# Performance work log

Measured on AMD Instinct MI355X. Metric: run time of the kernel, lower is better.

Reference implementation:

```python
import jax, jax.numpy as jnp
import numpy as np

N_NODES = 100000
N_EDGES = 1600000
IN_C, HID_C, OUT_C = 512, 128, 40


def gcn_conv(x, edge_index):
    """Symmetric-normalized sparse aggregation: out[d] = sum_e 1/sqrt(deg[s]*deg[d]) * x[s]."""
    n = x.shape[0]
    src, dst = edge_index[0], edge_index[1]
    deg = jax.ops.segment_sum(jnp.ones_like(dst, dtype=x.dtype), dst, num_segments=n)
    deg = jnp.maximum(deg, 1.0)  # guard isolated nodes
    dinv = jax.lax.rsqrt(deg)
    w = dinv[src] * dinv[dst]                      # [E]
    msg = x[src] * w[:, None]                      # [E, C] gather + scale
    return jax.ops.segment_sum(msg, dst, num_segments=n)  # scatter-add -> [N, C]


def setup_inputs() -> dict:
    key = jax.random.key(0)
    k1, k2, k3, k4 = jax.random.split(key, 4)
    x = jax.random.normal(k1, (N_NODES, IN_C), dtype=jnp.float32)
    edge_index = jax.random.randint(k2, (2, N_EDGES), 0, N_NODES, dtype=jnp.int64)
    # xavier_uniform with gain=1.414 (as in reset_parameters), zero biases
    def xavier(k, shape, gain=1.414):
        fan_out, fan_in = shape
        bound = gain * np.sqrt(6.0 / (fan_in + fan_out))
        return jax.random.uniform(k, shape, jnp.float32, -bound, bound)
    W0 = xavier(k3, (HID_C, IN_C))
    b0 = jnp.zeros((HID_C,), jnp.float32)
    W1 = xavier(k4, (OUT_C, HID_C))
    b1 = jnp.zeros((OUT_C,), jnp.float32)
    return {"x": x, "edge_index": edge_index, "W0": W0, "b0": b0, "W1": W1, "b1": b1}


def reference(x, edge_index, W0, b0, W1, b1):
    # layer 0: project -> sparse aggregate -> bias -> relu (dropout off in eval)
    h = x @ W0.T
    h = gcn_conv(h, edge_index)
    h = jax.nn.relu(h + b0)
    # final layer: project -> sparse aggregate -> bias (no activation)
    h = h @ W1.T
    h = gcn_conv(h, edge_index)
    return h + b1
```

## Files before the change

kernel.cpp:

```cpp
#include <hip/hip_runtime.h>
#include <hip/hip_bf16.h>
#include <cstddef>

#define N_NODES 100000
#define N_EDGES 1600000
#define IN_C 512
#define HID_C 128
#define OUT_C 40
#define OUT_CP 48
#define EPB 8000
#define NPART 200
#define NBKT 196
#define BSHIFT 9

typedef short bf16x8 __attribute__((ext_vector_type(8)));
typedef float f32x4 __attribute__((ext_vector_type(4)));

__device__ __forceinline__ float bf2f(unsigned short u) {
    union { unsigned int i; float f; } v; v.i = ((unsigned int)u) << 16; return v.f;
}
__device__ __forceinline__ float bf2f_lo(unsigned int u) {
    union { unsigned int i; float f; } v; v.i = u << 16; return v.f;
}
__device__ __forceinline__ float bf2f_hi(unsigned int u) {
    union { unsigned int i; float f; } v; v.i = u & 0xFFFF0000u; return v.f;
}
__device__ __forceinline__ unsigned short f2bf(float f) {
    union { float f; unsigned int i; } v; v.f = f;
    unsigned int x = v.i;
    return (unsigned short)((x + 0x7FFFu + ((x >> 16) & 1u)) >> 16);
}

__device__ __forceinline__ void glds16(const void* g, void* l) {
    __builtin_amdgcn_global_load_lds(
        (const __attribute__((address_space(1))) unsigned int*)g,
        (__attribute__((address_space(3))) unsigned int*)l,
        16, 0, 0);
}

__global__ void k_detect(const unsigned int* __restrict__ xbits,
                         const int* __restrict__ ei32, int* __restrict__ flags) {
    int lane = threadIdx.x & 63;
    unsigned int b = xbits[lane * 33 + 1];
    int e = (int)((b >> 23) & 0xFFu);
    unsigned long long bal = __ballot(e >= 90 && e <= 160);
    int zpred = (lane < 8) ? (ei32[2 * lane + 1] == 0) : 0;
    unsigned long long zb = __ballot(zpred);
    if (lane == 0) {
        flags[0] = (__popcll(bal) >= 32) ? 0 : 1;
        flags[1] = ((zb & 0xFFull) == 0xFFull) ? 1 : 0;
    }
}

__device__ __forceinline__ int load_src(const int* ei, int mi, int e) {
    return mi ? ei[2 * e] : ei[e];
}
__device__ __forceinline__ int load_dst(const int* ei, int mi, int e) {
    return mi ? ei[2 * (N_EDGES + e)] : ei[N_EDGES + e];
}

#define NW_TOTAL (IN_C * HID_C + HID_C * OUT_C + HID_C + OUT_C)
__global__ void k_norm_w(const void* __restrict__ W0, const void* __restrict__ W1,
                         const void* __restrict__ b0, const void* __restrict__ b1,
                         const int* __restrict__ flags,
                         unsigned short* __restrict__ w0n, unsigned short* __restrict__ w1n,
                         float* __restrict__ b0n, float* __restrict__ b1n) {
    int mf = flags[0];
    int i = blockIdx.x * 256 + threadIdx.x;
    if (i >= NW_TOTAL) return;
    if (i < IN_C * HID_C) {
        w0n[i] = mf ? ((const unsigned short*)W0)[i] : f2bf(((const float*)W0)[i]);
    } else if (i < IN_C * HID_C + HID_C * OUT_C) {
        int j = i - IN_C * HID_C;
        w1n[j] = mf ? ((const unsigned short*)W1)[j] : f2bf(((const float*)W1)[j]);
    } else if (i < IN_C * HID_C + HID_C * OUT_C + HID_C) {
        int j = i - IN_C * HID_C - HID_C * OUT_C;
        b0n[j] = mf ? bf2f(((const unsigned short*)b0)[j]) : ((const float*)b0)[j];
    } else {
        int j = i - IN_C * HID_C - HID_C * OUT_C - HID_C;
        b1n[j] = mf ? bf2f(((const unsigned short*)b1)[j]) : ((const float*)b1)[j];
    }
}

__global__ __launch_bounds__(256) void k_part1(const int* __restrict__ ei,
                                               const int* __restrict__ flags,
                                               int* __restrict__ bcnt,
                                               int* __restrict__ block_off) {
    __shared__ int h[NBKT];
    int t = threadIdx.x;
    for (int i = t; i < NBKT; i += 256) h[i] = 0;
    __syncthreads();
    int mi = flags[1];
    int base = blockIdx.x * EPB;
    for (int j = t; j < EPB; j += 256) {
        int e = base + j;
        if (e < N_EDGES) atomicAdd(&h[load_dst(ei, mi, e) >> BSHIFT], 1);
    }
    __syncthreads();
    for (int i = t; i < NBKT; i += 256)
        block_off[blockIdx.x * NBKT + i] = atomicAdd(&bcnt[i], h[i]);
}

__global__ void k_scan_bkt(const int* __restrict__ bcnt, int* __restrict__ bbase) {
    __shared__ int sm[256];
    int t = threadIdx.x;
    int v = (t < NBKT) ? bcnt[t] : 0;
    sm[t] = v; __syncthreads();
    for (int off = 1; off < 256; off <<= 1) {
        int a = (t >= off) ? sm[t - off] : 0;
        __syncthreads();
        sm[t] += a;
        __syncthreads();
    }
    if (t < NBKT) bbase[t] = sm[t] - v;
    if (t == NBKT - 1) bbase[NBKT] = sm[t];
}

__global__ __launch_bounds__(256) void k_part2(const int* __restrict__ ei,
                                               const int* __restrict__ flags,
                                               const int* __restrict__ bbase,
                                               const int* __restrict__ block_off,
                                               unsigned int* __restrict__ bedges) {
    __shared__ int cur[NBKT];
    int t = threadIdx.x;
    for (int i = t; i < NBKT; i += 256)
        cur[i] = bbase[i] + block_off[blockIdx.x * NBKT + i];
    __syncthreads();
    int mi = flags[1];
    int base = blockIdx.x * EPB;
    for (int j = t; j < EPB; j += 256) {
        int e = base + j;
        if (e < N_EDGES) {
            int d = load_dst(ei, mi, e);
            int s = load_src(ei, mi, e);
            int p = atomicAdd(&cur[d >> BSHIFT], 1);
            bedges[p] = ((unsigned int)s << BSHIFT) | (unsigned int)(d & 511);
        }
    }
}

__global__ __launch_bounds__(512) void k_bucket_csr(const unsigned int* __restrict__ bedges,
                                                    const int* __restrict__ bbase,
                                                    int* __restrict__ rowptr,
                                                    float* __restrict__ dinv,
                                                    int* __restrict__ col) {
    __shared__ int cnt[512];
    __shared__ int cur[512];
    int b = blockIdx.x, t = threadIdx.x;
    int ebeg = bbase[b], eend = bbase[b + 1];
    cnt[t] = 0;
    __syncthreads();
    for (int j = ebeg + t; j < eend; j += 512)
        atomicAdd(&cnt[bedges[j] & 511], 1);
    __syncthreads();
    int v = cnt[t];
    cur[t] = v; __syncthreads();
    for (int off = 1; off < 512; off <<= 1) {
        int a = (t >= off) ? cur[t - off] : 0;
        __syncthreads();
        cur[t] += a;
        __syncthreads();
    }
    int excl = cur[t] - v;
    int node = b * 512 + t;
    if (node < N_NODES) {
        rowptr[node] = ebeg + excl;
        float dd = (float)v; if (dd < 1.f) dd = 1.f;
        dinv[node] = rsqrtf(dd);
    } else if (node == N_NODES) {
        rowptr[N_NODES] = ebeg + excl;
    }
    __syncthreads();
    cur[t] = ebeg + excl;
    __syncthreads();
    for (int j = ebeg + t; j < eend; j += 512) {
        unsigned int pk = bedges[j];
        int p = atomicAdd(&cur[pk & 511], 1);
        col[p] = (int)(pk >> BSHIFT);
    }
}

#define G1_BUF 24576
#define G1_BOFF 16384

__device__ __forceinline__ void gemm1_f32_async(const float* __restrict__ xg,
                                                const unsigned short* __restrict__ w0n,
                                                const float* __restrict__ dinv,
                                                unsigned short* __restrict__ h1,
                                                char* __restrict__ smem,
                                                int node0, int t) {
    const int w = t >> 6;
    const int lane = t & 63;
    const int r16 = lane & 15;
    const int quad = lane >> 4;

    f32x4 acc[2][8];
#pragma unroll
    for (int m = 0; m < 2; m++)
#pragma unroll
        for (int c = 0; c < 8; c++) acc[m][c] = (f32x4){0.f, 0.f, 0.f, 0.f};

    const int lrow = lane >> 3;
    const int lch = (lane & 7) ^ lrow;
    const float* pa[4];
#pragma unroll
    for (int g = 0; g < 4; g++) {
        int r = node0 + w * 32 + 8 * g + lrow;
        if (r >= N_NODES) r = N_NODES - 1;
        pa[g] = xg + (size_t)r * IN_C + lch * 4;
    }
    const unsigned short* pb[2];
#pragma unroll
    for (int g = 0; g < 2; g++)
        pb[g] = w0n + (size_t)((2 * w + g) * 16 + r16) * IN_C + quad * 8;

    auto stage = [&](int buf, int ks) {
        char* Ab = smem + buf * G1_BUF + w * 4096;
        char* Bb = smem + buf * G1_BUF + G1_BOFF + w * 2048;
        glds16(pa[0] + ks, Ab);
        glds16(pa[1] + ks, Ab + 1024);
        glds16(pa[2] + ks, Ab + 2048);
        glds16(pa[3] + ks, Ab + 3072);
        glds16(pb[0] + ks, Bb);
        glds16(pb[1] + ks, Bb + 1024);
    };

    const int swz = r16 & 7;

    auto compute = [&](int buf) {
        const char* Ab = smem + buf * G1_BUF;
        const char* Bb = Ab + G1_BOFF;
        bf16x8 a[2];
#pragma unroll
        for (int m = 0; m < 2; m++) {
            int rowb = (w * 32 + m * 16 + r16) * 128;
            int c0 = ((2 * quad) ^ swz) * 16;
            int c1 = ((2 * quad + 1) ^ swz) * 16;
            float4 fa = *reinterpret_cast<const float4*>(Ab + rowb + c0);
            float4 fb = *reinterpret_cast<const float4*>(Ab + rowb + c1);
            a[m] = (bf16x8){(short)f2bf(fa.x), (short)f2bf(fa.y), (short)f2bf(fa.z), (short)f2bf(fa.w),
                            (short)f2bf(fb.x), (short)f2bf(fb.y), (short)f2bf(fb.z), (short)f2bf(fb.w)};
        }
#pragma unroll
        for (int ct = 0; ct < 8; ct++) {
            bf16x8 b = *reinterpret_cast<const bf16x8*>(Bb + ct * 1024 + lane * 16);
            acc[0][ct] = __builtin_amdgcn_mfma_f32_16x16x32_bf16(a[0], b, acc[0][ct], 0, 0, 0);
            acc[1][ct] = __builtin_amdgcn_mfma_f32_16x16x32_bf16(a[1], b, acc[1][ct], 0, 0, 0);
        }
    };

    stage(0, 0);
    stage(1, 32);
    for (int tt = 0; tt < 14; ++tt) {
        asm volatile("s_waitcnt vmcnt(6)" ::: "memory");
        __builtin_amdgcn_sched_barrier(0);
        __builtin_amdgcn_s_barrier();
        compute(tt & 1);
        __builtin_amdgcn_s_barrier();
        stage(tt & 1, (tt + 2) * 32);
    }
    asm volatile("s_waitcnt vmcnt(6)" ::: "memory");
    __builtin_amdgcn_sched_barrier(0);
    __builtin_amdgcn_s_barrier();
    compute(0);
    asm volatile("s_waitcnt vmcnt(0)" ::: "memory");
    __builtin_amdgcn_sched_barrier(0);
    __builtin_amdgcn_s_barrier();
    compute(1);

#pragma unroll
    for (int m = 0; m < 2; m++) {
#pragma unroll
        for (int r = 0; r < 4; r++) {
            int row = node0 + w * 32 + m * 16 + quad * 4 + r;
            if (row < N_NODES) {
                float dv = dinv[row];
#pragma unroll
                for (int ct = 0; ct < 8; ct++)
                    h1[(size_t)row * HID_C + ct * 16 + r16] = f2bf(acc[m][ct][r] * dv);
            }
        }
    }
}

__device__ __forceinline__ void gemm1_bf16_async(const unsigned short* __restrict__ xg,
                                                 const unsigned short* __restrict__ w0n,
                                                 const float* __restrict__ dinv,
                                                 unsigned short* __restrict__ h1,
                                                 unsigned short* __restrict__ smem,
                                                 int node0, int t) {
    const int w = t >> 6;
    const int lane = t & 63;
    const int r16 = lane & 15;
    const int quad = lane >> 4;

    f32x4 acc[2][8];
#pragma unroll
    for (int m = 0; m < 2; m++)
#pragma unroll
        for (int c = 0; c < 8; c++) acc[m][c] = (f32x4){0.f, 0.f, 0.f, 0.f};

    int rA0 = node0 + (2 * w) * 16 + r16;     if (rA0 >= N_NODES) rA0 = N_NODES - 1;
    int rA1 = node0 + (2 * w + 1) * 16 + r16; if (rA1 >= N_NODES) rA1 = N_NODES - 1;
    const unsigned short* pa0 = xg + (size_t)rA0 * IN_C + quad * 8;
    const unsigned short* pa1 = xg + (size_t)rA1 * IN_C + quad * 8;
    const unsigned short* pb0 = w0n + (size_t)((2 * w) * 16 + r16) * IN_C + quad * 8;
    const unsigned short* pb1 = w0n + (size_t)((2 * w + 1) * 16 + r16) * IN_C + quad * 8;

    auto stage = [&](int buf, int ks) {
        unsigned short* a = smem + buf * 8192 + (2 * w) * 512;
        glds16(pa0 + ks, a);
        glds16(pa1 + ks, a + 512);
        glds16(pb0 + ks, a + 4096);
        glds16(pb1 + ks, a + 4096 + 512);
    };

    const int fo = quad * 128 + r16 * 8;

    auto compute = [&](int buf) {
        const unsigned short* Ab = smem + buf * 8192;
        const unsigned short* Bb = Ab + 4096;
        bf16x8 a0 = *reinterpret_cast<const bf16x8*>(Ab + (2 * w) * 512 + fo);
        bf16x8 a1 = *reinterpret_cast<const bf16x8*>(Ab + (2 * w + 1) * 512 + fo);
#pragma unroll
        for (int ct = 0; ct < 8; ct++) {
            bf16x8 b = *reinterpret_cast<const bf16x8*>(Bb + ct * 512 + fo);
            acc[0][ct] = __builtin_amdgcn_mfma_f32_16x16x32_bf16(a0, b, acc[0][ct], 0, 0, 0);
            acc[1][ct] = __builtin_amdgcn_mfma_f32_16x16x32_bf16(a1, b, acc[1][ct], 0, 0, 0);
        }
    };

    stage(0, 0);
    __syncthreads();
    for (int tt = 0; tt < 15; ++tt) {
        int cur = tt & 1;
        stage(cur ^ 1, (tt + 1) * 32);
        compute(cur);
        __syncthreads();
    }
    compute(1);

#pragma unroll
    for (int m = 0; m < 2; m++) {
#pragma unroll
        for (int r = 0; r < 4; r++) {
            int row = node0 + w * 32 + m * 16 + quad * 4 + r;
            if (row < N_NODES) {
                float dv = dinv[row];
#pragma unroll
                for (int ct = 0; ct < 8; ct++)
                    h1[(size_t)row * HID_C + ct * 16 + r16] = f2bf(acc[m][ct][r] * dv);
            }
        }
    }
}

__global__ __launch_bounds__(256, 3) void k_gemm1(const void* __restrict__ x,
                                                  const unsigned short* __restrict__ w0n,
                                                  const int* __restrict__ flags,
                                                  const float* __restrict__ dinv,
                                                  unsigned short* __restrict__ h1) {
    __shared__ __align__(16) char smem[2 * G1_BUF];
    int node0 = blockIdx.x * 128;
    int t = threadIdx.x;
    if (flags[0]) gemm1_bf16_async((const unsigned short*)x, w0n, dinv, h1,
                                   (unsigned short*)smem, node0, t);
    else          gemm1_f32_async((const float*)x, w0n, dinv, h1, smem, node0, t);
}

__global__ __launch_bounds__(256) void k_agg1g2(const int* __restrict__ rowptr,
                                                const int* __restrict__ col,
                                                const float* __restrict__ dinv,
                                                const unsigned int* __restrict__ h1v,
                                                const float* __restrict__ b0n,
                                                const unsigned short* __restrict__ w1p,
                                                float* __restrict__ p2) {
    __shared__ unsigned int H[16][68];
    int w = threadIdx.x >> 6;
    int lane = threadIdx.x & 63;
    int nb = blockIdx.x * 16;
    float bl = b0n[2 * lane], bh = b0n[2 * lane + 1];
#pragma unroll
    for (int i = 0; i < 4; i++) {
        int d = nb + w * 4 + i;
        int beg = __builtin_amdgcn_readfirstlane(rowptr[d]);
        int end = __builtin_amdgcn_readfirstlane(rowptr[d + 1]);
        float a0 = 0.f, a1 = 0.f;
        for (int j0 = beg; j0 < end; j0 += 16) {
            int s[16];
            float m[16];
#pragma unroll
            for (int q = 0; q < 16; q++) {
                int jj = j0 + q;
                int jc = jj < end ? jj : end - 1;
                s[q] = col[jc];
                m[q] = jj < end ? 1.f : 0.f;
            }
            unsigned int r[16];
#pragma unroll
            for (int q = 0; q < 16; q++) {
                const unsigned int* rp = h1v + (size_t)s[q] * 64;
                r[q] = rp[lane];
            }
#pragma unroll
            for (int q = 0; q < 16; q++) {
                a0 += m[q] * bf2f_lo(r[q]);
                a1 += m[q] * bf2f_hi(r[q]);
            }
        }
        float dv = dinv[d];
        float o0 = a0 * dv + bl;
        float o1 = a1 * dv + bh;
        o0 = o0 > 0.f ? o0 : 0.f;
        o1 = o1 > 0.f ? o1 : 0.f;
        H[w * 4 + i][lane] = (unsigned int)f2bf(o0) | ((unsigned int)f2bf(o1) << 16);
    }
    __syncthreads();
    if (w != 0) return;

    int r16 = lane & 15;
    int quad = lane >> 4;
    f32x4 acc[3];
#pragma unroll
    for (int c = 0; c < 3; c++) acc[c] = (f32x4){0.f, 0.f, 0.f, 0.f};

    const unsigned short* brow = w1p + (size_t)r16 * HID_C + quad * 8;
#pragma unroll
    for (int k0 = 0; k0 < HID_C; k0 += 32) {
        bf16x8 a = *reinterpret_cast<const bf16x8*>(&H[r16][k0 / 2 + quad * 4]);
#pragma unroll
        for (int ct = 0; ct < 3; ct++) {
            bf16x8 b = *reinterpret_cast<const bf16x8*>(brow + (size_t)ct * 16 * HID_C + k0);
            acc[ct] = __builtin_amdgcn_mfma_f32_16x16x32_bf16(a, b, acc[ct], 0, 0, 0);
        }
    }

    float dvv[4];
#pragma unroll
    for (int r = 0; r < 4; r++) dvv[r] = dinv[nb + quad * 4 + r];

#pragma unroll
    for (int ct = 0; ct < 3; ct++) {
        int chan = ct * 16 + r16;
        if (chan < OUT_C) {
#pragma unroll
            for (int r = 0; r < 4; r++) {
                p2[(size_t)(nb + quad * 4 + r) * OUT_C + chan] = acc[ct][r] * dvv[r];
            }
        }
    }
}

__global__ __launch_bounds__(256) void k_agg2(const int* __restrict__ rowptr,
                                              const int* __restrict__ col,
                                              const float* __restrict__ dinv,
                                              const float* __restrict__ p2,
                                              const float* __restrict__ b1n,
                                              const int* __restrict__ flags,
                                              void* __restrict__ out) {
    int w = threadIdx.x >> 6;
    int lane = threadIdx.x & 63;
    int d = blockIdx.x * 4 + w;
    if (d >= N_NODES || lane >= OUT_C) return;
    int beg = __builtin_amdgcn_readfirstlane(rowptr[d]);
    int end = __builtin_amdgcn_readfirstlane(rowptr[d + 1]);
    float acc = 0.f;
    for (int j0 = beg; j0 < end; j0 += 16) {
        int s[16];
        float m[16];
#pragma unroll
        for (int q = 0; q < 16; q++) {
            int jj = j0 + q;
            int jc = jj < end ? jj : end - 1;
            s[q] = col[jc];
            m[q] = jj < end ? 1.f : 0.f;
        }
        float r[16];
#pragma unroll
        for (int q = 0; q < 16; q++) {
            const float* rp = p2 + (size_t)s[q] * OUT_C;
            r[q] = rp[lane];
        }
#pragma unroll
        for (int q = 0; q < 16; q++) acc += m[q] * r[q];
    }
    float v = acc * dinv[d] + b1n[lane];
    size_t idx = (size_t)d * OUT_C + lane;
    if (flags[0]) ((unsigned short*)out)[idx] = f2bf(v);
    else          ((float*)out)[idx] = v;
}

extern "C" void kernel_launch(void* const* d_in, const int* in_sizes, int n_in,
                              void* d_out, int out_size, void* d_ws, size_t ws_size,
                              hipStream_t stream) {
    const void* x  = d_in[0];
    const int* ei  = (const int*)d_in[1];
    const void* W0 = d_in[2];
    const void* b0 = d_in[3];
    const void* W1 = d_in[4];
    const void* b1 = d_in[5];

    char* ws = (char*)d_ws;
    size_t off = 0;
    auto alloc = [&](size_t bytes) {
        char* p = ws + off;
        off += (bytes + 511) & ~(size_t)511;
        return p;
    };
    int*   flags   = (int*)  alloc(sizeof(int) * 2);
    int*   rowptr  = (int*)  alloc(sizeof(int) * (N_NODES + 1));
    float* dinv    = (float*)alloc(sizeof(float) * N_NODES);
    int*   col     = (int*)  alloc(sizeof(int) * N_EDGES);
    int*   bcnt    = (int*)  alloc(sizeof(int) * NBKT);
    int*   bbase   = (int*)  alloc(sizeof(int) * (NBKT + 1));
    int*   bloff   = (int*)  alloc(sizeof(int) * NPART * NBKT);
    unsigned int* bedges = (unsigned int*)alloc(sizeof(unsigned int) * N_EDGES);
    unsigned short* w0n = (unsigned short*)alloc(sizeof(unsigned short) * IN_C * HID_C);
    unsigned short* w1n = (unsigned short*)alloc(sizeof(unsigned short) * OUT_CP * HID_C);
    float* b0n = (float*)alloc(sizeof(float) * HID_C);
    float* b1n = (float*)alloc(sizeof(float) * OUT_C);
    unsigned short* h1 = (unsigned short*)alloc(sizeof(unsigned short) * (size_t)N_NODES * HID_C);
    float* p2 = (float*)alloc(sizeof(float) * (size_t)N_NODES * OUT_C);

    k_detect<<<1, 64, 0, stream>>>((const unsigned int*)x, ei, flags);
    hipMemsetAsync(w1n, 0, sizeof(unsigned short) * OUT_CP * HID_C, stream);
    k_norm_w<<<(NW_TOTAL + 255) / 256, 256, 0, stream>>>(W0, W1, b0, b1, flags, w0n, w1n, b0n, b1n);

    hipMemsetAsync(bcnt, 0, sizeof(int) * NBKT, stream);
    k_part1<<<NPART, 256, 0, stream>>>(ei, flags, bcnt, bloff);
    k_scan_bkt<<<1, 256, 0, stream>>>(bcnt, bbase);
    k_part2<<<NPART, 256, 0, stream>>>(ei, flags, bbase, bloff, bedges);
    k_bucket_csr<<<NBKT, 512, 0, stream>>>(bedges, bbase, rowptr, dinv, col);

    k_gemm1<<<(N_NODES + 127) / 128, 256, 0, stream>>>(x, w0n, flags, dinv, h1);
    k_agg1g2<<<N_NODES / 16, 256, 0, stream>>>(rowptr, col, dinv,
                                               (const unsigned int*)h1, b0n,
                                               w1n, p2);
    k_agg2<<<(N_NODES + 3) / 4, 256, 0, stream>>>(rowptr, col, dinv, p2, b1n, flags, d_out);
}
```

Baseline: 493.4 us.

## Split gemm1 over output column halves, keep W0 slice resident in LDS

The first projection GEMM now launches two blocks per 128-row tile, each computing 64 output channels. Each block loads its full 64x512 bf16 slice of W0 into swizzled LDS once, then streams A operands straight from global memory into registers with a one-step software prefetch. This drops the double-buffered LDS staging of A and the per-step barriers. The trade-off is that each block rereads its x rows (fp32 or bf16) from global memory, doubling x traffic unless L2 absorbs it. It also uses 64 KB of LDS per block, so launch bounds drop to two blocks per CU.

```diff
diff --git a/kernel.cpp b/kernel.cpp
--- a/kernel.cpp
+++ b/kernel.cpp
@@ -12,6 +12,7 @@
 #define NPART 200
 #define NBKT 196
 #define BSHIFT 9
+#define G1_ROWBLK 782
 
 typedef short bf16x8 __attribute__((ext_vector_type(8)));
 typedef float f32x4 __attribute__((ext_vector_type(4)));
@@ -29,6 +30,10 @@
     union { float f; unsigned int i; } v; v.f = f;
     unsigned int x = v.i;
     return (unsigned short)((x + 0x7FFFu + ((x >> 16) & 1u)) >> 16);
+}
+__device__ __forceinline__ bf16x8 pack8(float4 a, float4 b) {
+    return (bf16x8){(short)f2bf(a.x), (short)f2bf(a.y), (short)f2bf(a.z), (short)f2bf(a.w),
+                    (short)f2bf(b.x), (short)f2bf(b.y), (short)f2bf(b.z), (short)f2bf(b.w)};
 }
 
 __device__ __forceinline__ void glds16(const void* g, void* l) {
@@ -180,93 +185,91 @@
     }
 }
 
-#define G1_BUF 24576
-#define G1_BOFF 16384
-
-__device__ __forceinline__ void gemm1_f32_async(const float* __restrict__ xg,
-                                                const unsigned short* __restrict__ w0n,
-                                                const float* __restrict__ dinv,
-                                                unsigned short* __restrict__ h1,
-                                                char* __restrict__ smem,
-                                                int node0, int t) {
+__device__ __forceinline__ const bf16x8* ldsB(const unsigned short* Bs, int row,
+                                              int s, int quad) {
+    int ch = (4 * s + quad) ^ (row & 7);
+    return reinterpret_cast<const bf16x8*>(
+        (const char*)Bs + row * 1024 + ch * 16);
+}
+
+template <int MF>
+__device__ __forceinline__ void gemm1_body(const void* __restrict__ x,
+                                           const unsigned short* __restrict__ w0n,
+                                           const float* __restrict__ dinv,
+                                           unsigned short* __restrict__ h1,
+                                           unsigned short* __restrict__ Bs,
+                                           int node0, int chb, int t) {
     const int w = t >> 6;
     const int lane = t & 63;
     const int r16 = lane & 15;
     const int quad = lane >> 4;
 
-    f32x4 acc[2][8];
+    {
+        const unsigned short* src = w0n + (size_t)(chb + 16 * w) * IN_C;
+        unsigned short* dst = Bs + (size_t)(16 * w) * 512;
+#pragma unroll
+        for (int g = 0; g < 16; g++) {
+            glds16(src + (size_t)g * 512 + (size_t)(lane ^ (g & 7)) * 8,
+                   dst + (size_t)g * 512);
+        }
+    }
+
+    f32x4 acc[2][4];
 #pragma unroll
     for (int m = 0; m < 2; m++)
 #pragma unroll
-        for (int c = 0; c < 8; c++) acc[m][c] = (f32x4){0.f, 0.f, 0.f, 0.f};
-
-    const int lrow = lane >> 3;
-    const int lch = (lane & 7) ^ lrow;
-    const float* pa[4];
-#pragma unroll
-    for (int g = 0; g < 4; g++) {
-        int r = node0 + w * 32 + 8 * g + lrow;
-        if (r >= N_NODES) r = N_NODES - 1;
-        pa[g] = xg + (size_t)r * IN_C + lch * 4;
-    }
-    const unsigned short* pb[2];
-#pragma unroll
-    for (int g = 0; g < 2; g++)
-        pb[g] = w0n + (size_t)((2 * w + g) * 16 + r16) * IN_C + quad * 8;
-
-    auto stage = [&](int buf, int ks) {
-        char* Ab = smem + buf * G1_BUF + w * 4096;
-        char* Bb = smem + buf * G1_BUF + G1_BOFF + w * 2048;
-        glds16(pa[0] + ks, Ab);
-        glds16(pa[1] + ks, Ab + 1024);
-        glds16(pa[2] + ks, Ab + 2048);
-        glds16(pa[3] + ks, Ab + 3072);
-        glds16(pb[0] + ks, Bb);
-        glds16(pb[1] + ks, Bb + 1024);
-    };
-
-    const int swz = r16 & 7;
-
-    auto compute = [&](int buf) {
-        const char* Ab = smem + buf * G1_BUF;
-        const char* Bb = Ab + G1_BOFF;
-        bf16x8 a[2];
-#pragma unroll
-        for (int m = 0; m < 2; m++) {
-            int rowb = (w * 32 + m * 16 + r16) * 128;
-            int c0 = ((2 * quad) ^ swz) * 16;
-            int c1 = ((2 * quad + 1) ^ swz) * 16;
-            float4 fa = *reinterpret_cast<const float4*>(Ab + rowb + c0);
-            float4 fb = *reinterpret_cast<const float4*>(Ab + rowb + c1);
-            a[m] = (bf16x8){(short)f2bf(fa.x), (short)f2bf(fa.y), (short)f2bf(fa.z), (short)f2bf(fa.w),
-                            (short)f2bf(fb.x), (short)f2bf(fb.y), (short)f2bf(fb.z), (short)f2bf(fb.w)};
-        }
-#pragma unroll
-        for (int ct = 0; ct < 8; ct++) {
-            bf16x8 b = *reinterpret_cast<const bf16x8*>(Bb + ct * 1024 + lane * 16);
-            acc[0][ct] = __builtin_amdgcn_mfma_f32_16x16x32_bf16(a[0], b, acc[0][ct], 0, 0, 0);
-            acc[1][ct] = __builtin_amdgcn_mfma_f32_16x16x32_bf16(a[1], b, acc[1][ct], 0, 0, 0);
-        }
-    };
-
-    stage(0, 0);
-    stage(1, 32);
-    for (int tt = 0; tt < 14; ++tt) {
-        asm volatile("s_waitcnt vmcnt(6)" ::: "memory");
-        __builtin_amdgcn_sched_barrier(0);
-        __builtin_amdgcn_s_barrier();
-        compute(tt & 1);
-        __builtin_amdgcn_s_barrier();
-        stage(tt & 1, (tt + 2) * 32);
-    }
-    asm volatile("s_waitcnt vmcnt(6)" ::: "memory");
-    __builtin_amdgcn_sched_barrier(0);
-    __builtin_amdgcn_s_barrier();
-    compute(0);
-    asm volatile("s_waitcnt vmcnt(0)" ::: "memory");
-    __builtin_amdgcn_sched_barrier(0);
-    __builtin_amdgcn_s_barrier();
-    compute(1);
+        for (int c = 0; c < 4; c++) acc[m][c] = (f32x4){0.f, 0.f, 0.f, 0.f};
+
+    int r0 = node0 + w * 32 + r16;      int r0c = r0 < N_NODES ? r0 : N_NODES - 1;
+    int r1 = r0 + 16;                   int r1c = r1 < N_NODES ? r1 : N_NODES - 1;
+    const float* a0f = (const float*)x + (size_t)r0c * IN_C + quad * 8;
+    const float* a1f = (const float*)x + (size_t)r1c * IN_C + quad * 8;
+    const unsigned short* a0h = (const unsigned short*)x + (size_t)r0c * IN_C + quad * 8;
+    const unsigned short* a1h = (const unsigned short*)x + (size_t)r1c * IN_C + quad * 8;
+
+    __syncthreads();
+
+    if (MF) {
+        bf16x8 c0 = *reinterpret_cast<const bf16x8*>(a0h);
+        bf16x8 c1 = *reinterpret_cast<const bf16x8*>(a1h);
+#pragma unroll
+        for (int s = 0; s < 16; s++) {
+            int sn = (s < 15) ? s + 1 : s;
+            bf16x8 n0 = *reinterpret_cast<const bf16x8*>(a0h + 32 * sn);
+            bf16x8 n1 = *reinterpret_cast<const bf16x8*>(a1h + 32 * sn);
+#pragma unroll
+            for (int ct = 0; ct < 4; ct++) {
+                bf16x8 b = *ldsB(Bs, ct * 16 + r16, s, quad);
+                acc[0][ct] = __builtin_amdgcn_mfma_f32_16x16x32_bf16(c0, b, acc[0][ct], 0, 0, 0);
+                acc[1][ct] = __builtin_amdgcn_mfma_f32_16x16x32_bf16(c1, b, acc[1][ct], 0, 0, 0);
+            }
+            c0 = n0; c1 = n1;
+        }
+    } else {
+        float4 c00 = *reinterpret_cast<const float4*>(a0f);
+        float4 c01 = *reinterpret_cast<const float4*>(a0f + 4);
+        float4 c10 = *reinterpret_cast<const float4*>(a1f);
+        float4 c11 = *reinterpret_cast<const float4*>(a1f + 4);
+#pragma unroll
+        for (int s = 0; s < 16; s++) {
+            int sn = (s < 15) ? s + 1 : s;
+            const float* p0 = a0f + 32 * sn;
+            const float* p1 = a1f + 32 * sn;
+            float4 n00 = *reinterpret_cast<const float4*>(p0);
+            float4 n01 = *reinterpret_cast<const float4*>(p0 + 4);
+            float4 n10 = *reinterpret_cast<const float4*>(p1);
+            float4 n11 = *reinterpret_cast<const float4*>(p1 + 4);
+            bf16x8 av0 = pack8(c00, c01);
+            bf16x8 av1 = pack8(c10, c11);
+#pragma unroll
+            for (int ct = 0; ct < 4; ct++) {
+                bf16x8 b = *ldsB(Bs, ct * 16 + r16, s, quad);
+                acc[0][ct] = __builtin_amdgcn_mfma_f32_16x16x32_bf16(av0, b, acc[0][ct], 0, 0, 0);
+                acc[1][ct] = __builtin_amdgcn_mfma_f32_16x16x32_bf16(av1, b, acc[1][ct], 0, 0, 0);
+            }
+            c00 = n00; c01 = n01; c10 = n10; c11 = n11;
+        }
+    }
 
 #pragma unroll
     for (int m = 0; m < 2; m++) {
@@ -276,96 +279,24 @@
             if (row < N_NODES) {
                 float dv = dinv[row];
 #pragma unroll
-                for (int ct = 0; ct < 8; ct++)
-                    h1[(size_t)row * HID_C + ct * 16 + r16] = f2bf(acc[m][ct][r] * dv);
-            }
-        }
-    }
-}
-
-__device__ __forceinline__ void gemm1_bf16_async(const unsigned short* __restrict__ xg,
-                                                 const unsigned short* __restrict__ w0n,
-                                                 const float* __restrict__ dinv,
-                                                 unsigned short* __restrict__ h1,
-                                                 unsigned short* __restrict__ smem,
-                                                 int node0, int t) {
-    const int w = t >> 6;
-    const int lane = t & 63;
-    const int r16 = lane & 15;
-    const int quad = lane >> 4;
-
-    f32x4 acc[2][8];
-#pragma unroll
-    for (int m = 0; m < 2; m++)
-#pragma unroll
-        for (int c = 0; c < 8; c++) acc[m][c] = (f32x4){0.f, 0.f, 0.f, 0.f};
-
-    int rA0 = node0 + (2 * w) * 16 + r16;     if (rA0 >= N_NODES) rA0 = N_NODES - 1;
-    int rA1 = node0 + (2 * w + 1) * 16 + r16; if (rA1 >= N_NODES) rA1 = N_NODES - 1;
-    const unsigned short* pa0 = xg + (size_t)rA0 * IN_C + quad * 8;
-    const unsigned short* pa1 = xg + (size_t)rA1 * IN_C + quad * 8;
-    const unsigned short* pb0 = w0n + (size_t)((2 * w) * 16 + r16) * IN_C + quad * 8;
-    const unsigned short* pb1 = w0n + (size_t)((2 * w + 1) * 16 + r16) * IN_C + quad * 8;
-
-    auto stage = [&](int buf, int ks) {
-        unsigned short* a = smem + buf * 8192 + (2 * w) * 512;
-        glds16(pa0 + ks, a);
-        glds16(pa1 + ks, a + 512);
-        glds16(pb0 + ks, a + 4096);
-        glds16(pb1 + ks, a + 4096 + 512);
-    };
-
-    const int fo = quad * 128 + r16 * 8;
-
-    auto compute = [&](int buf) {
-        const unsigned short* Ab = smem + buf * 8192;
-        const unsigned short* Bb = Ab + 4096;
-        bf16x8 a0 = *reinterpret_cast<const bf16x8*>(Ab + (2 * w) * 512 + fo);
-        bf16x8 a1 = *reinterpret_cast<const bf16x8*>(Ab + (2 * w + 1) * 512 + fo);
-#pragma unroll
-        for (int ct = 0; ct < 8; ct++) {
-            bf16x8 b = *reinterpret_cast<const bf16x8*>(Bb + ct * 512 + fo);
-            acc[0][ct] = __builtin_amdgcn_mfma_f32_16x16x32_bf16(a0, b, acc[0][ct], 0, 0, 0);
-            acc[1][ct] = __builtin_amdgcn_mfma_f32_16x16x32_bf16(a1, b, acc[1][ct], 0, 0, 0);
-        }
-    };
-
-    stage(0, 0);
-    __syncthreads();
-    for (int tt = 0; tt < 15; ++tt) {
-        int cur = tt & 1;
-        stage(cur ^ 1, (tt + 1) * 32);
-        compute(cur);
-        __syncthreads();
-    }
-    compute(1);
-
-#pragma unroll
-    for (int m = 0; m < 2; m++) {
-#pragma unroll
-        for (int r = 0; r < 4; r++) {
-            int row = node0 + w * 32 + m * 16 + quad * 4 + r;
-            if (row < N_NODES) {
-                float dv = dinv[row];
-#pragma unroll
-                for (int ct = 0; ct < 8; ct++)
-                    h1[(size_t)row * HID_C + ct * 16 + r16] = f2bf(acc[m][ct][r] * dv);
-            }
-        }
-    }
-}
-
-__global__ __launch_bounds__(256, 3) void k_gemm1(const void* __restrict__ x,
+                for (int ct = 0; ct < 4; ct++)
+                    h1[(size_t)row * HID_C + chb + ct * 16 + r16] = f2bf(acc[m][ct][r] * dv);
+            }
+        }
+    }
+}
+
+__global__ __launch_bounds__(256, 2) void k_gemm1(const void* __restrict__ x,
                                                   const unsigned short* __restrict__ w0n,
                                                   const int* __restrict__ flags,
                                                   const float* __restrict__ dinv,
                                                   unsigned short* __restrict__ h1) {
-    __shared__ __align__(16) char smem[2 * G1_BUF];
-    int node0 = blockIdx.x * 128;
+    __shared__ __align__(16) unsigned short Bs[64 * IN_C];
+    int node0 = ((int)blockIdx.x >> 1) * 128;
+    int chb = ((int)blockIdx.x & 1) * 64;
     int t = threadIdx.x;
-    if (flags[0]) gemm1_bf16_async((const unsigned short*)x, w0n, dinv, h1,
-                                   (unsigned short*)smem, node0, t);
-    else          gemm1_f32_async((const float*)x, w0n, dinv, h1, smem, node0, t);
+    if (flags[0]) gemm1_body<1>(x, w0n, dinv, h1, Bs, node0, chb, t);
+    else          gemm1_body<0>(x, w0n, dinv, h1, Bs, node0, chb, t);
 }
 
 __global__ __launch_bounds__(256) void k_agg1g2(const int* __restrict__ rowptr,
@@ -532,7 +463,7 @@
     k_part2<<<NPART, 256, 0, stream>>>(ei, flags, bbase, bloff, bedges);
     k_bucket_csr<<<NBKT, 512, 0, stream>>>(bedges, bbase, rowptr, dinv, col);
 
-    k_gemm1<<<(N_NODES + 127) / 128, 256, 0, stream>>>(x, w0n, flags, dinv, h1);
+    k_gemm1<<<2 * G1_ROWBLK, 256, 0, stream>>>(x, w0n, flags, dinv, h1);
     k_agg1g2<<<N_NODES / 16, 256, 0, stream>>>(rowptr, col, dinv,
                                                (const unsigned int*)h1, b0n,
                                                w1n, p2);
```

After: 517.2 us. 4.8% more time.
